# Optimization experiments

Measured on AMD Instinct MI355X. Metric: run time of the kernel, lower is better.

The kernel has to match this reference:

```python
import jax, jax.numpy as jnp
import numpy as np
from functools import partial

D_MODEL = 1024
D_STATE = 16
D_CONV = 4
EXPAND = 2
DIM = EXPAND * D_MODEL  # 2048


def setup_inputs() -> dict:
    key = jax.random.key(0)
    ks = jax.random.split(key, 10)
    s = lambda fan_in: 1.0 / np.sqrt(fan_in)
    inp = {
        "x": jax.random.normal(ks[0], (8, 2048, D_MODEL), dtype=jnp.float32),
        "W_in": jax.random.normal(ks[1], (DIM, D_MODEL), dtype=jnp.float32) * s(D_MODEL),
        "b_in": jnp.zeros((DIM,), dtype=jnp.float32),
        "conv_w": jax.random.normal(ks[2], (DIM, 1, D_CONV), dtype=jnp.float32) * s(D_CONV),
        "conv_b": jnp.zeros((DIM,), dtype=jnp.float32),
        "W_x": jax.random.normal(ks[3], (3 * D_STATE, DIM), dtype=jnp.float32) * s(DIM),
        "W_dt": jax.random.normal(ks[4], (DIM, D_STATE), dtype=jnp.float32) * s(D_STATE),
        "b_dt": jnp.zeros((DIM,), dtype=jnp.float32),
        "W_out": jax.random.normal(ks[5], (D_MODEL, DIM), dtype=jnp.float32) * s(DIM),
        "b_out": jnp.zeros((D_MODEL,), dtype=jnp.float32),
    }
    return inp


def _selective_scan(xc, delta, A, Bm, Cm):
    # xc, delta: (B, L, DIM); Bm, Cm: (B, L, N); A: (N,)
    Bsz = xc.shape[0]
    h0 = jnp.zeros((Bsz, DIM, D_STATE), dtype=xc.dtype)

    def step(h, inputs):
        xc_t, d_t, b_t, c_t = inputs  # (B,DIM),(B,DIM),(B,N),(B,N)
        h = h * jnp.exp(d_t[:, :, None] * A) + xc_t[:, :, None] * b_t[:, None, :]
        y_t = jnp.einsum("bdn,bn->bd", h, c_t)
        return h, y_t

    tm = lambda a: jnp.swapaxes(a, 0, 1)  # time-major
    _, ys = jax.lax.scan(step, h0, (tm(xc), tm(delta), tm(Bm), tm(Cm)))
    return jnp.swapaxes(ys, 0, 1)  # (B, L, DIM)


def reference(x, W_in, b_in, conv_w, conv_b, W_x, W_dt, b_dt, W_out, b_out):
    A = -jnp.exp(jnp.linspace(0.0, -5.0, D_STATE).astype(x.dtype))  # (N,)
    xp = x @ W_in.T + b_in  # (B, L, DIM)
    # depthwise conv1d, padding=D_CONV-1 on BOTH sides (as torch Conv1d) -> length L+D_CONV-1
    xc = jax.lax.conv_general_dilated(
        jnp.swapaxes(xp, 1, 2), conv_w,
        window_strides=(1,), padding=[(D_CONV - 1, D_CONV - 1)],
        feature_group_count=DIM,
        dimension_numbers=("NCH", "OIH", "NCH"),
    ) + conv_b[None, :, None]
    xc = jnp.swapaxes(xc, 1, 2)  # (B, Lc, DIM)
    x_dbl = xc @ W_x.T  # (B, Lc, 3N)
    d_raw, Bm, Cm = jnp.split(x_dbl, [D_STATE, 2 * D_STATE], axis=-1)
    delta = jax.nn.softplus(d_raw @ W_dt.T + b_dt)  # (B, Lc, DIM)
    y = _selective_scan(xc, delta, A, Bm, Cm)  # (B, Lc, DIM)
    return y @ W_out.T + b_out  # (B, Lc, D_MODEL)
```

## Files before the change

### kernel.cpp

```cpp
#include <hip/hip_runtime.h>
#include <cstdint>
#include <cstddef>

#define B8 8
#define LSEQ 2048
#define LC 2051
#define DMODEL 1024
#define DIM 2048
#define LPAD 2054
#define M2 16408
#define M2P 16512
#define CS 32
#define NCH 65

typedef __attribute__((ext_vector_type(8))) short short8;
typedef __attribute__((ext_vector_type(4))) float floatx4;
typedef __attribute__((ext_vector_type(2))) float float2v;
typedef __attribute__((address_space(3))) unsigned short lds_ushort;

__device__ __constant__ float AeT[16] = {
  -1.0f,          -0.71653131f, -0.51341712f, -0.36787944f,
  -0.26359714f,   -0.18887560f, -0.13533528f, -0.09697208f,
  -0.06948345f,   -0.04978707f, -0.03567399f, -0.02556154f,
  -0.01831564f,   -0.01312373f, -0.00940356f, -0.00673795f};

#define LOG2E 1.44269504088896f

__device__ __forceinline__ float bf2f(unsigned short h) {
  union { unsigned int u; float f; } v; v.u = ((unsigned int)h) << 16; return v.f;
}
__device__ __forceinline__ unsigned short f2bf(float f) {
  union { float f; unsigned int u; } v; v.f = f;
  unsigned int r = (v.u + 0x7FFFu + ((v.u >> 16) & 1u)) >> 16;
  return (unsigned short)r;
}

__device__ __forceinline__ float2v pk_mul_vv(float2v a, float2v b) {
  float2v d; asm("v_pk_mul_f32 %0, %1, %2" : "=v"(d) : "v"(a), "v"(b)); return d;
}
__device__ __forceinline__ float2v pk_mul_sv(float2v bs, float2v a) {
  float2v d; asm("v_pk_mul_f32 %0, %1, %2" : "=v"(d) : "s"(bs), "v"(a)); return d;
}
__device__ __forceinline__ float2v pk_fma_vvv(float2v a, float2v b, float2v c) {
  float2v d; asm("v_pk_fma_f32 %0, %1, %2, %3" : "=v"(d) : "v"(a), "v"(b), "v"(c)); return d;
}
__device__ __forceinline__ float2v pk_fma_vsv(float2v a, float2v bs, float2v c) {
  float2v d; asm("v_pk_fma_f32 %0, %1, %2, %3" : "=v"(d) : "v"(a), "s"(bs), "v"(c)); return d;
}
__device__ __forceinline__ float2v pk_add_vv(float2v a, float2v b) {
  float2v d; asm("v_pk_add_f32 %0, %1, %2" : "=v"(d) : "v"(a), "v"(b)); return d;
}
__device__ __forceinline__ float exp2_raw(float x) {
  float d; asm("v_exp_f32 %0, %1" : "=v"(d) : "v"(x)); return d;
}

__device__ __forceinline__ short8 ds_read_b128_(const lds_ushort* p) {
  floatx4 d;
  unsigned addr = (unsigned)(size_t)p;
  asm volatile("ds_read_b128 %0, %1" : "=v"(d) : "v"(addr));
  return __builtin_bit_cast(short8, d);
}

__global__ __launch_bounds__(256) void init_kernel(const float* __restrict__ x,
                                                   const float* __restrict__ W_in,
                                                   const float* __restrict__ W_out,
                                                   const float* __restrict__ W_x,
                                                   unsigned short* __restrict__ xA,
                                                   unsigned short* __restrict__ wInB,
                                                   unsigned short* __restrict__ wOutB,
                                                   unsigned short* __restrict__ wXB,
                                                   unsigned short* __restrict__ xp) {
  const int gid = blockIdx.x;
  const float* in; unsigned short* out; int i;
  if (gid < 8192)        { in = x;     out = xA;    i = gid * 256 + threadIdx.x; }
  else if (gid < 9216)   { in = W_in;  out = wInB;  i = (gid - 8192) * 256 + threadIdx.x; }
  else if (gid < 10240)  { in = W_out; out = wOutB; i = (gid - 9216) * 256 + threadIdx.x; }
  else if (gid < 10288)  { in = W_x;   out = wXB;   i = (gid - 10240) * 256 + threadIdx.x; }
  else {
    int ii = (gid - 10288) * 256 + threadIdx.x;
    int b = ii / 1536;
    int r6 = (ii % 1536) / 256;
    int dd = (ii % 256) * 8;
    int row = (r6 < 3) ? r6 : (2048 + r6);
    *(uint4*)(xp + ((size_t)b * LPAD + row) * DIM + dd) = make_uint4(0, 0, 0, 0);
    return;
  }
  const float4* p = (const float4*)in + (size_t)i * 2;
  float4 a = p[0], b = p[1];
  uint4 o;
  o.x = (unsigned)f2bf(a.x) | ((unsigned)f2bf(a.y) << 16);
  o.y = (unsigned)f2bf(a.z) | ((unsigned)f2bf(a.w) << 16);
  o.z = (unsigned)f2bf(b.x) | ((unsigned)f2bf(b.y) << 16);
  o.w = (unsigned)f2bf(b.z) | ((unsigned)f2bf(b.w) << 16);
  *((uint4*)out + i) = o;
}

__global__ __launch_bounds__(256) void conv_kernel(const unsigned short* __restrict__ xp,
                                                   const float* __restrict__ conv_w,
                                                   const float* __restrict__ conv_b,
                                                   unsigned short* __restrict__ xc) {
  const int tc0 = blockIdx.x * 16;
  const int b = blockIdx.y;
  const int d0 = threadIdx.x * 8;

  float4 cw[8];
#pragma unroll
  for (int j = 0; j < 8; ++j) cw[j] = *(const float4*)(conv_w + (size_t)(d0 + j) * 4);
  float cb[8];
  {
    const float4* cb4 = (const float4*)(conv_b + d0);
    float4 c0 = cb4[0], c1 = cb4[1];
    cb[0] = c0.x; cb[1] = c0.y; cb[2] = c0.z; cb[3] = c0.w;
    cb[4] = c1.x; cb[5] = c1.y; cb[6] = c1.z; cb[7] = c1.w;
  }

  const unsigned short* base = xp + ((size_t)b * LPAD + tc0) * DIM + d0;
  unsigned short* outp = xc + ((size_t)b * LC + tc0) * DIM + d0;

  auto loadrow = [&](float (&w)[8], int r) {
    uint4 v = *(const uint4*)(base + (size_t)r * DIM);
    w[0] = bf2f(v.x & 0xffff); w[1] = bf2f(v.x >> 16);
    w[2] = bf2f(v.y & 0xffff); w[3] = bf2f(v.y >> 16);
    w[4] = bf2f(v.z & 0xffff); w[5] = bf2f(v.z >> 16);
    w[6] = bf2f(v.w & 0xffff); w[7] = bf2f(v.w >> 16);
  };

  float wa[8], wb[8], wc[8];
  loadrow(wa, 0); loadrow(wb, 1); loadrow(wc, 2);
#pragma unroll
  for (int i = 0; i < 16; ++i) {
    float wd[8];
    loadrow(wd, i + 3);
    if (tc0 + i < LC) {
      float acc[8];
#pragma unroll
      for (int j = 0; j < 8; ++j) {
        acc[j] = cb[j];
        acc[j] = fmaf(wa[j], cw[j].x, acc[j]);
        acc[j] = fmaf(wb[j], cw[j].y, acc[j]);
        acc[j] = fmaf(wc[j], cw[j].z, acc[j]);
        acc[j] = fmaf(wd[j], cw[j].w, acc[j]);
      }
      uint4 o;
      o.x = (unsigned)f2bf(acc[0]) | ((unsigned)f2bf(acc[1]) << 16);
      o.y = (unsigned)f2bf(acc[2]) | ((unsigned)f2bf(acc[3]) << 16);
      o.z = (unsigned)f2bf(acc[4]) | ((unsigned)f2bf(acc[5]) << 16);
      o.w = (unsigned)f2bf(acc[6]) | ((unsigned)f2bf(acc[7]) << 16);
      *(uint4*)(outp + (size_t)i * DIM) = o;
    }
#pragma unroll
    for (int j = 0; j < 8; ++j) { wa[j] = wb[j]; wb[j] = wc[j]; wc[j] = wd[j]; }
  }
}

#define GAS(p) ((const __attribute__((address_space(1))) void*)(p))
#define LAS(p) ((__attribute__((address_space(3))) void*)(p))

template <int MODE, int NBM, int NBN, int LX, int TAIL>
__global__ __launch_bounds__(256) void gemm_bt(const unsigned short* __restrict__ A,
                                               const unsigned short* __restrict__ Bw,
                                               const float* __restrict__ bias,
                                               void* __restrict__ Cout, int K) {
  const int gid = blockIdx.x;
  const int mainBlocks = 8 * LX * NBN;
  int bm, bn;
  if (TAIL && gid >= mainBlocks) {
    const int e = gid - mainBlocks;
    bm = 8 * LX + e / NBN;
    bn = e % NBN;
  } else {
    const int xcd = gid & 7;
    const int j = gid >> 3;
    bm = xcd * LX + (j % LX);
    bn = j / LX;
  }
  if (bm >= NBM) return;

  __shared__ __align__(16) unsigned short As[2][128 * 64];
  __shared__ __align__(16) unsigned short Bs[2][128 * 64];
  const int tid = threadIdx.x;
  const int lane = tid & 63, wave = tid >> 6;
  const int wr = wave >> 1, wc = wave & 1;

  floatx4 acc[4][4];
#pragma unroll
  for (int i = 0; i < 4; ++i)
#pragma unroll
    for (int j2 = 0; j2 < 4; ++j2) acc[i][j2] = (floatx4){0.f, 0.f, 0.f, 0.f};

  const int srow = tid >> 3;
  const int scol = ((tid & 7) ^ ((tid >> 3) & 7)) * 8;
  const unsigned short* Ab[4];
  const unsigned short* Bb[4];
#pragma unroll
  for (int L = 0; L < 4; ++L) {
    Ab[L] = A  + (size_t)(bm * 128 + L * 32 + srow) * K + scol;
    Bb[L] = Bw + (size_t)(bn * 128 + L * 32 + srow) * K + scol;
  }

  const int fr = lane & 15;
  const int hi = lane >> 4;
  const int fx = fr & 7;

  auto STAGE = [&](int buf, int k0) {
#pragma unroll
    for (int L = 0; L < 4; ++L) {
      __builtin_amdgcn_global_load_lds(GAS(Ab[L] + k0), LAS(&As[buf][L * 2048 + tid * 8]), 16, 0, 0);
      __builtin_amdgcn_global_load_lds(GAS(Bb[L] + k0), LAS(&Bs[buf][L * 2048 + tid * 8]), 16, 0, 0);
    }
  };

  const int NT = K >> 6;
  STAGE(0, 0);
  asm volatile("s_waitcnt vmcnt(0)");
  __syncthreads();

  int cur = 0;
  for (int t = 0; t < NT; ++t) {
    if (t + 1 < NT) STAGE(cur ^ 1, (t + 1) * 64);

    const lds_ushort* tA = (const lds_ushort*)LAS(&As[cur][0]);
    const lds_ushort* tB = (const lds_ushort*)LAS(&Bs[cur][0]);
#pragma unroll
    for (int kk = 0; kk < 2; ++kk) {
      const int pb = ((kk * 4 + hi) ^ fx) * 8;
      short8 af[4], bf[4];
#pragma unroll
      for (int mt = 0; mt < 4; ++mt) af[mt] = ds_read_b128_(tA + (wr * 64 + mt * 16 + fr) * 64 + pb);
#pragma unroll
      for (int nt = 0; nt < 4; ++nt) bf[nt] = ds_read_b128_(tB + (wc * 64 + nt * 16 + fr) * 64 + pb);
      asm volatile("s_waitcnt lgkmcnt(0)");
      __builtin_amdgcn_sched_barrier(0);
      __builtin_amdgcn_s_setprio(1);
#pragma unroll
      for (int mt = 0; mt < 4; ++mt)
#pragma unroll
        for (int nt = 0; nt < 4; ++nt)
          acc[mt][nt] = __builtin_amdgcn_mfma_f32_16x16x32_bf16(af[mt], bf[nt], acc[mt][nt], 0, 0, 0);
      __builtin_amdgcn_s_setprio(0);
    }
    __syncthreads();
    cur ^= 1;
  }

  const int er = (lane >> 4) * 4, ec = lane & 15;
#pragma unroll
  for (int mt = 0; mt < 4; ++mt) {
#pragma unroll
    for (int nt = 0; nt < 4; ++nt) {
#pragma unroll
      for (int i = 0; i < 4; ++i) {
        int r = bm * 128 + wr * 64 + mt * 16 + er + i;
        int c = bn * 128 + wc * 64 + nt * 16 + ec;
        float v = acc[mt][nt][i];
        if constexpr (MODE == 0) {
          int bb = r >> 11, t = r & 2047;
          ((unsigned short*)Cout)[((size_t)bb * LPAD + 3 + t) * DIM + c] = f2bf(v + bias[c]);
        } else if constexpr (MODE == 1) {
          if (r < M2 && c < 48) ((float*)Cout)[(size_t)r * 48 + c] = v;
        } else {
          if (r < M2) ((float*)Cout)[(size_t)r * DMODEL + c] = v + bias[c];
        }
      }
    }
  }
}

__global__ __launch_bounds__(256) void delta_kernel(const float* __restrict__ xdbl,
                                                    const float* __restrict__ W_dt,
                                                    const float* __restrict__ b_dt,
                                                    unsigned short* __restrict__ delta) {
  const int d = blockIdx.y * 256 + threadIdx.x;
  const int r0 = blockIdx.x * 8;
  float wv[16];
  const float4* wp = (const float4*)(W_dt + (size_t)d * 16);
#pragma unroll
  for (int q = 0; q < 4; ++q) {
    float4 t = wp[q];
    wv[q * 4 + 0] = t.x; wv[q * 4 + 1] = t.y; wv[q * 4 + 2] = t.z; wv[q * 4 + 3] = t.w;
  }
  const float bd = b_dt[d];
#pragma unroll
  for (int j = 0; j < 8; ++j) {
    const float* dr = xdbl + (size_t)(r0 + j) * 48;
    float z0 = bd, z1 = 0.f, z2 = 0.f, z3 = 0.f;
#pragma unroll
    for (int n = 0; n < 16; n += 4) {
      z0 = fmaf(dr[n + 0], wv[n + 0], z0);
      z1 = fmaf(dr[n + 1], wv[n + 1], z1);
      z2 = fmaf(dr[n + 2], wv[n + 2], z2);
      z3 = fmaf(dr[n + 3], wv[n + 3], z3);
    }
    float z = (z0 + z1) + (z2 + z3);
    float dl = (z > 20.f) ? z : __logf(1.f + __expf(z));
    delta[(size_t)(r0 + j) * DIM + d] = f2bf(dl);
  }
}

__global__ __launch_bounds__(256) void scan_pass1(const unsigned short* __restrict__ xc,
                                                  const unsigned short* __restrict__ dl,
                                                  const float* __restrict__ xd,
                                                  unsigned short* __restrict__ sdbuf,
                                                  unsigned short* __restrict__ qbuf) {
  const int wid = __builtin_amdgcn_readfirstlane((int)(threadIdx.x >> 6));
  const int lane = threadIdx.x & 63;
  const int W = blockIdx.x * 4 + wid;
  const int dg = W & 31;
  const int rest = W >> 5;
  const int c = rest % NCH;
  const int b = rest / NCH;
  const int d = dg * 64 + lane;
  const int t0 = c * CS;
  const int nst = (t0 + CS <= LC) ? CS : (LC - t0);

  float2v A2L[8];
#pragma unroll
  for (int i = 0; i < 8; ++i)
    A2L[i] = (float2v){AeT[2 * i] * LOG2E, AeT[2 * i + 1] * LOG2E};

  float2v h2[8];
#pragma unroll
  for (int i = 0; i < 8; ++i) h2[i] = (float2v){0.f, 0.f};
  float sumd = 0.f;

  const size_t row0 = (size_t)b * LC + t0;
  const float* xdb = xd + row0 * 48 + 16;
  const unsigned short* xcp = xc + row0 * DIM + d;
  const unsigned short* dp  = dl + row0 * DIM + d;

  auto body = [&](int s) {
    float2v Bv[8];
#pragma unroll
    for (int j = 0; j < 8; ++j) Bv[j] = *(const float2v*)(xdb + (size_t)s * 48 + 2 * j);
    float dlt = bf2f(dp[(size_t)s * DIM]);
    float xcv = bf2f(xcp[(size_t)s * DIM]);
    sumd += dlt;
    float2v dlt2 = (float2v){dlt, dlt};
    float2v xcv2 = (float2v){xcv, xcv};
#pragma unroll
    for (int i = 0; i < 8; ++i) {
      float2v arg = pk_mul_vv(dlt2, A2L[i]);
      float e0 = exp2_raw(arg.x), e1 = exp2_raw(arg.y);
      float2v e2 = (float2v){e0, e1};
      h2[i] = pk_fma_vvv(h2[i], e2, pk_mul_sv(Bv[i], xcv2));
    }
  };

  if (nst == CS) {
#pragma unroll
    for (int s = 0; s < CS; ++s) body(s);
  } else {
    for (int s = 0; s < nst; ++s) body(s);
  }

  sdbuf[((size_t)(b * NCH + c) << 11) + d] = f2bf(sumd);
  const size_t base = ((size_t)(b * NCH + c) * 16) * 2048 + d;
#pragma unroll
  for (int i = 0; i < 8; ++i) {
    qbuf[base + ((size_t)(2 * i) << 11)]     = f2bf(h2[i].x);
    qbuf[base + ((size_t)(2 * i + 1) << 11)] = f2bf(h2[i].y);
  }
}

__global__ __launch_bounds__(256) void scan_boundary(const unsigned short* __restrict__ sdbuf,
                                                     unsigned short* __restrict__ qbuf) {
  const int tid = threadIdx.x;
  const int n = tid >> 4;
  const int d = blockIdx.x * 16 + (tid & 15);
  const int b = blockIdx.y;
  const float aL = AeT[n] * LOG2E;
  float h = 0.f;
  for (int c = 0; c < NCH; ++c) {
    const size_t sbase = ((size_t)(b * NCH + c) << 11);
    const float sd = bf2f(sdbuf[sbase + d]);
    const size_t base = (sbase << 4) + ((size_t)n << 11) + d;
    const float qv = bf2f(qbuf[base]);
    const float Pv = exp2_raw(sd * aL);
    qbuf[base] = f2bf(h);
    h = fmaf(Pv, h, qv);
  }
}

__global__ __launch_bounds__(256) void scan_pass2(const unsigned short* __restrict__ xc,
                                                  const unsigned short* __restrict__ dl,
                                                  const float* __restrict__ xd,
                                                  const unsigned short* __restrict__ hinit,
                                                  unsigned short* __restrict__ y) {
  const int wid = __builtin_amdgcn_readfirstlane((int)(threadIdx.x >> 6));
  const int lane = threadIdx.x & 63;
  const int W = blockIdx.x * 4 + wid;
  const int dg = W & 31;
  const int rest = W >> 5;
  const int c = rest % NCH;
  const int b = rest / NCH;
  const int d = dg * 64 + lane;
  const int t0 = c * CS;
  const int nst = (t0 + CS <= LC) ? CS : (LC - t0);

  float2v A2L[8];
#pragma unroll
  for (int i = 0; i < 8; ++i)
    A2L[i] = (float2v){AeT[2 * i] * LOG2E, AeT[2 * i + 1] * LOG2E};

  const size_t base = ((size_t)(b * NCH + c) * 16) * 2048 + d;
  float2v h2[8];
#pragma unroll
  for (int i = 0; i < 8; ++i)
    h2[i] = (float2v){bf2f(hinit[base + ((size_t)(2 * i) << 11)]),
                      bf2f(hinit[base + ((size_t)(2 * i + 1) << 11)])};

  const size_t row0 = (size_t)b * LC + t0;
  const float* xdb = xd + row0 * 48 + 16;
  const unsigned short* xcp = xc + row0 * DIM + d;
  const unsigned short* dp  = dl + row0 * DIM + d;
  unsigned short* yp = y + row0 * DIM + d;

  auto body = [&](int s) {
    float2v Bv[8], Cv[8];
#pragma unroll
    for (int j = 0; j < 8; ++j) {
      Bv[j] = *(const float2v*)(xdb + (size_t)s * 48 + 2 * j);
      Cv[j] = *(const float2v*)(xdb + (size_t)s * 48 + 16 + 2 * j);
    }
    float dlt = bf2f(dp[(size_t)s * DIM]);
    float xcv = bf2f(xcp[(size_t)s * DIM]);
    float2v dlt2 = (float2v){dlt, dlt};
    float2v xcv2 = (float2v){xcv, xcv};
    float2v y2[4];
#pragma unroll
    for (int i = 0; i < 4; ++i) y2[i] = (float2v){0.f, 0.f};
#pragma unroll
    for (int i = 0; i < 8; ++i) {
      float2v arg = pk_mul_vv(dlt2, A2L[i]);
      float e0 = exp2_raw(arg.x), e1 = exp2_raw(arg.y);
      float2v e2 = (float2v){e0, e1};
      h2[i] = pk_fma_vvv(h2[i], e2, pk_mul_sv(Bv[i], xcv2));
      y2[i & 3] = pk_fma_vsv(h2[i], Cv[i], y2[i & 3]);
    }
    float2v s01 = pk_add_vv(y2[0], y2[1]);
    float2v s23 = pk_add_vv(y2[2], y2[3]);
    float2v st = pk_add_vv(s01, s23);
    yp[(size_t)s * DIM] = f2bf(st.x + st.y);
  };

  if (nst == CS) {
#pragma unroll
    for (int s = 0; s < CS; ++s) body(s);
  } else {
    for (int s = 0; s < nst; ++s) body(s);
  }
}

extern "C" void kernel_launch(void* const* d_in, const int* in_sizes, int n_in,
                              void* d_out, int out_size, void* d_ws, size_t ws_size,
                              hipStream_t stream) {
  const float* x      = (const float*)d_in[0];
  const float* W_in   = (const float*)d_in[1];
  const float* b_in   = (const float*)d_in[2];
  const float* conv_w = (const float*)d_in[3];
  const float* conv_b = (const float*)d_in[4];
  const float* W_x    = (const float*)d_in[5];
  const float* W_dt   = (const float*)d_in[6];
  const float* b_dt   = (const float*)d_in[7];
  const float* W_out  = (const float*)d_in[8];
  const float* b_out  = (const float*)d_in[9];

  char* w = (char*)d_ws;
  unsigned short* xp    = (unsigned short*)w;
  unsigned short* delta = (unsigned short*)w;
  unsigned short* ybuf  = (unsigned short*)w;
  size_t off = (size_t)M2P * DIM * 2;
  unsigned short* xcb  = (unsigned short*)(w + off); off += (size_t)M2P * DIM * 2;
  size_t xA_off = off;
  unsigned short* xA   = (unsigned short*)(w + off); off += (size_t)16384 * 1024 * 2;
  unsigned short* wInB = (unsigned short*)(w + off); off += (size_t)2048 * 1024 * 2;
  unsigned short* wOutB= (unsigned short*)(w + off); off += (size_t)1024 * 2048 * 2;
  unsigned short* wXB  = (unsigned short*)(w + off); off += (size_t)128 * 2048 * 2;
  float* xdbl          = (float*)(w + off);          off += (size_t)M2 * 48 * 4;
  unsigned short* sdbuf = (unsigned short*)(w + xA_off);
  unsigned short* qbuf  = (unsigned short*)(w + xA_off + (size_t)B8 * NCH * 2048 * 2);
  (void)ws_size; (void)in_sizes; (void)n_in; (void)out_size;

  init_kernel<<<10336, 256, 0, stream>>>(x, W_in, W_out, W_x, xA, wInB, wOutB, wXB, xp);

  gemm_bt<0, 128, 16, 16, 0><<<2048, 256, 0, stream>>>(xA, wInB, b_in, xp, 1024);
  conv_kernel<<<dim3(129, B8), 256, 0, stream>>>(xp, conv_w, conv_b, xcb);
  gemm_bt<1, 129, 1, 16, 1><<<129, 256, 0, stream>>>(xcb, wXB, nullptr, xdbl, 2048);
  delta_kernel<<<dim3(2051, 8), 256, 0, stream>>>(xdbl, W_dt, b_dt, delta);

  scan_pass1<<<4160, 256, 0, stream>>>(xcb, delta, xdbl, sdbuf, qbuf);
  scan_boundary<<<dim3(128, B8), 256, 0, stream>>>(sdbuf, qbuf);
  scan_pass2<<<4160, 256, 0, stream>>>(xcb, delta, xdbl, qbuf, ybuf);

  gemm_bt<2, 129, 8, 16, 1><<<1032, 256, 0, stream>>>(ybuf, wOutB, b_out, (float*)d_out, 2048);
}
```

Baseline: 521.2 us.

## Split-K the x_dbl projection GEMM across eight blocks with a reduction kernel

The x_dbl GEMM (N=48, padded to 128, K=2048) previously launched only 129 blocks, leaving most CUs idle. It now splits K into eight slices for 1032 blocks, writes fp32 partials into a scratch region reused from the xA buffer, and adds a small kernel that sums the partials into xdbl. This trades an extra launch and partial-buffer traffic for much higher parallelism on a latency-bound GEMM.

```diff
diff --git a/kernel.cpp b/kernel.cpp
--- a/kernel.cpp
+++ b/kernel.cpp
@@ -156,15 +156,19 @@
 #define GAS(p) ((const __attribute__((address_space(1))) void*)(p))
 #define LAS(p) ((__attribute__((address_space(3))) void*)(p))
 
-template <int MODE, int NBM, int NBN, int LX, int TAIL>
+template <int MODE, int NBM, int NBN, int LX, int TAIL, int SPLITK>
 __global__ __launch_bounds__(256) void gemm_bt(const unsigned short* __restrict__ A,
                                                const unsigned short* __restrict__ Bw,
                                                const float* __restrict__ bias,
                                                void* __restrict__ Cout, int K) {
   const int gid = blockIdx.x;
   const int mainBlocks = 8 * LX * NBN;
-  int bm, bn;
-  if (TAIL && gid >= mainBlocks) {
+  int bm, bn, ks = 0;
+  if constexpr (SPLITK) {
+    ks = gid & 7;
+    bm = gid >> 3;
+    bn = 0;
+  } else if (TAIL && gid >= mainBlocks) {
     const int e = gid - mainBlocks;
     bm = 8 * LX + e / NBN;
     bn = e % NBN;
@@ -210,14 +214,15 @@
     }
   };
 
-  const int NT = K >> 6;
-  STAGE(0, 0);
+  const int kbase = SPLITK ? ks * (K >> 3) : 0;
+  const int NT = (SPLITK ? (K >> 3) : K) >> 6;
+  STAGE(0, kbase);
   asm volatile("s_waitcnt vmcnt(0)");
   __syncthreads();
 
   int cur = 0;
   for (int t = 0; t < NT; ++t) {
-    if (t + 1 < NT) STAGE(cur ^ 1, (t + 1) * 64);
+    if (t + 1 < NT) STAGE(cur ^ 1, kbase + (t + 1) * 64);
 
     const lds_ushort* tA = (const lds_ushort*)LAS(&As[cur][0]);
     const lds_ushort* tB = (const lds_ushort*)LAS(&Bs[cur][0]);
@@ -257,13 +262,26 @@
           int bb = r >> 11, t = r & 2047;
           ((unsigned short*)Cout)[((size_t)bb * LPAD + 3 + t) * DIM + c] = f2bf(v + bias[c]);
         } else if constexpr (MODE == 1) {
-          if (r < M2 && c < 48) ((float*)Cout)[(size_t)r * 48 + c] = v;
+          if (c < 48) ((float*)Cout)[((size_t)ks * M2P + r) * 48 + c] = v;
         } else {
           if (r < M2) ((float*)Cout)[(size_t)r * DMODEL + c] = v + bias[c];
         }
       }
     }
   }
+}
+
+__global__ __launch_bounds__(256) void reduce_xdbl(const float* __restrict__ part,
+                                                   float* __restrict__ xdbl) {
+  int i = blockIdx.x * 256 + threadIdx.x;
+  if (i >= 196896) return;
+  float4 s = make_float4(0.f, 0.f, 0.f, 0.f);
+#pragma unroll
+  for (int ks = 0; ks < 8; ++ks) {
+    float4 v = *(const float4*)(part + (size_t)ks * M2P * 48 + (size_t)i * 4);
+    s.x += v.x; s.y += v.y; s.z += v.z; s.w += v.w;
+  }
+  *(float4*)(xdbl + (size_t)i * 4) = s;
 }
 
 __global__ __launch_bounds__(256) void delta_kernel(const float* __restrict__ xdbl,
@@ -477,20 +495,22 @@
   unsigned short* wOutB= (unsigned short*)(w + off); off += (size_t)1024 * 2048 * 2;
   unsigned short* wXB  = (unsigned short*)(w + off); off += (size_t)128 * 2048 * 2;
   float* xdbl          = (float*)(w + off);          off += (size_t)M2 * 48 * 4;
+  float* part           = (float*)(w + xA_off);
   unsigned short* sdbuf = (unsigned short*)(w + xA_off);
   unsigned short* qbuf  = (unsigned short*)(w + xA_off + (size_t)B8 * NCH * 2048 * 2);
   (void)ws_size; (void)in_sizes; (void)n_in; (void)out_size;
 
   init_kernel<<<10336, 256, 0, stream>>>(x, W_in, W_out, W_x, xA, wInB, wOutB, wXB, xp);
 
-  gemm_bt<0, 128, 16, 16, 0><<<2048, 256, 0, stream>>>(xA, wInB, b_in, xp, 1024);
+  gemm_bt<0, 128, 16, 16, 0, 0><<<2048, 256, 0, stream>>>(xA, wInB, b_in, xp, 1024);
   conv_kernel<<<dim3(129, B8), 256, 0, stream>>>(xp, conv_w, conv_b, xcb);
-  gemm_bt<1, 129, 1, 16, 1><<<129, 256, 0, stream>>>(xcb, wXB, nullptr, xdbl, 2048);
+  gemm_bt<1, 129, 1, 0, 0, 1><<<1032, 256, 0, stream>>>(xcb, wXB, nullptr, part, 2048);
+  reduce_xdbl<<<770, 256, 0, stream>>>(part, xdbl);
   delta_kernel<<<dim3(2051, 8), 256, 0, stream>>>(xdbl, W_dt, b_dt, delta);
 
   scan_pass1<<<4160, 256, 0, stream>>>(xcb, delta, xdbl, sdbuf, qbuf);
   scan_boundary<<<dim3(128, B8), 256, 0, stream>>>(sdbuf, qbuf);
   scan_pass2<<<4160, 256, 0, stream>>>(xcb, delta, xdbl, qbuf, ybuf);
 
-  gemm_bt<2, 129, 8, 16, 1><<<1032, 256, 0, stream>>>(ybuf, wOutB, b_out, (float*)d_out, 2048);
-}
+  gemm_bt<2, 129, 8, 16, 1, 0><<<1032, 256, 0, stream>>>(ybuf, wOutB, b_out, (float*)d_out, 2048);
+}
```

Result: no change. 511.3 us (-1.9%).
